# Kernel tuning notes

Measured on AMD Instinct MI355X. Metric: run time of the kernel, lower is better.

## Reference

```python
import jax, jax.numpy as jnp
import numpy as np
import math

B, T, C, H = 2, 2048, 512, 8
K, DIL = 3, 1
EPS = 1e-5


def _ln(x, g, b):
    m = jnp.mean(x, axis=-1, keepdims=True)
    v = jnp.mean(jnp.square(x - m), axis=-1, keepdims=True)
    return (x - m) * jax.lax.rsqrt(v + EPS) * g + b


def setup_inputs() -> dict:
    key = jax.random.key(0)
    ks = jax.random.split(key, 12)
    s = 0.02
    return {
        "x": jax.random.normal(ks[0], (B, T, C), jnp.float32),
        "conv_w": jax.random.normal(ks[1], (C, C, K), jnp.float32) * s,  # OIH
        "conv_b": jax.random.normal(ks[2], (C,), jnp.float32) * s,
        "g1": jnp.ones((C,), jnp.float32), "b1": jnp.zeros((C,), jnp.float32),
        "qkv_w": jax.random.normal(ks[3], (C, 3 * C), jnp.float32) * s,
        "qkv_b": jax.random.normal(ks[4], (3 * C,), jnp.float32) * s,
        "proj_w": jax.random.normal(ks[5], (C, C), jnp.float32) * s,
        "proj_b": jax.random.normal(ks[6], (C,), jnp.float32) * s,
        "g2": jnp.ones((C,), jnp.float32), "b2": jnp.zeros((C,), jnp.float32),
        "ffn_w1": jax.random.normal(ks[7], (C, 2 * C), jnp.float32) * s,
        "ffn_b1": jax.random.normal(ks[8], (2 * C,), jnp.float32) * s,
        "ffn_w2": jax.random.normal(ks[9], (2 * C, C), jnp.float32) * s,
        "ffn_b2": jax.random.normal(ks[10], (C,), jnp.float32) * s,
        "g3": jnp.ones((C,), jnp.float32), "b3": jnp.zeros((C,), jnp.float32),
    }


def reference(x, conv_w, conv_b, g1, b1, qkv_w, qkv_b, proj_w, proj_b,
              g2, b2, ffn_w1, ffn_b1, ffn_w2, ffn_b2, g3, b3):
    b, t, c = x.shape
    hd = c // H
    # --- causal dilated conv (left-pad only == pad both + right-trim) ---
    pad = (K - 1) * DIL
    xc = jnp.transpose(x, (0, 2, 1))  # [B,C,T]
    conv = jax.lax.conv_general_dilated(
        xc, conv_w, window_strides=(1,), padding=[(pad, 0)],
        rhs_dilation=(DIL,), dimension_numbers=("NCH", "OIH", "NCH"))
    conv = conv + conv_b[None, :, None]
    x = _ln(x + jnp.transpose(conv, (0, 2, 1)), g1, b1)
    # --- causal self-attention ---
    qkv = (x @ qkv_w + qkv_b).reshape(b, t, 3, H, hd)
    qkv = jnp.transpose(qkv, (2, 0, 3, 1, 4))  # [3,B,H,T,hd]
    q, k, v = qkv[0], qkv[1], qkv[2]
    scores = jnp.einsum("bhqd,bhkd->bhqk", q, k) / math.sqrt(hd)
    causal = jnp.tril(jnp.ones((t, t), bool))
    scores = jnp.where(causal, scores, -jnp.inf)
    attn = jax.nn.softmax(scores, axis=-1)
    out = jnp.einsum("bhqk,bhkd->bhqd", attn, v)
    out = jnp.transpose(out, (0, 2, 1, 3)).reshape(b, t, c)
    out = out @ proj_w + proj_b
    x = _ln(x + out, g2, b2)
    # --- FFN ---
    ffn = jax.nn.relu(x @ ffn_w1 + ffn_b1) @ ffn_w2 + ffn_b2
    return _ln(x + ffn, g3, b3)
```

## Files before the change

### kernel.cpp

```cpp
#include <hip/hip_runtime.h>
#include <hip/hip_bf16.h>

#define TT 2048
#define QSC 0.18033688011112042f

typedef __attribute__((ext_vector_type(4))) float f32x4;
typedef __attribute__((ext_vector_type(8))) __bf16 bf16x8;
typedef __attribute__((ext_vector_type(4))) short short4v;
typedef __attribute__((ext_vector_type(8))) short short8v;

enum { M_CONV = 0, M_QKV = 1, M_PROJ = 2, M_FFN1 = 3, M_FFN2 = 4 };

__device__ __forceinline__ void gload16(const void* g, void* l) {
    __builtin_amdgcn_global_load_lds(
        (__attribute__((address_space(1))) void*)g,
        (__attribute__((address_space(3))) void*)l, 16, 0, 0);
}

__device__ __forceinline__ short f2bf(float f) {
    unsigned u = __float_as_uint(f);
    u = (u + 0x7fffu + ((u >> 16) & 1u)) >> 16;
    return (short)u;
}

__device__ __forceinline__ float bf2f(short s) {
    unsigned u = ((unsigned)(unsigned short)s) << 16;
    return __uint_as_float(u);
}

__global__ __launch_bounds__(256) void prep_all(
    const float* __restrict__ conv_w, const float* __restrict__ x,
    const float* __restrict__ qkv_w, const float* __restrict__ proj_w,
    const float* __restrict__ f1w, const float* __restrict__ f2w,
    short* __restrict__ cwT, short* __restrict__ xpad,
    short* __restrict__ qkvT, short* __restrict__ projT,
    short* __restrict__ f1T, short* __restrict__ f2T) {
    if (blockIdx.x < 2048) {
        int t = blockIdx.x;
        const float* src; short* dst; int K, N, lt;
        if (t < 768)       { src = qkv_w;  dst = qkvT;  K = 512;  N = 1536; lt = t; }
        else if (t < 1024) { src = proj_w; dst = projT; K = 512;  N = 512;  lt = t - 768; }
        else if (t < 1536) { src = f1w;    dst = f1T;   K = 512;  N = 1024; lt = t - 1024; }
        else               { src = f2w;    dst = f2T;   K = 1024; N = 512;  lt = t - 1536; }
        int ntn = N >> 5;
        int kt = lt / ntn, nt = lt - kt * ntn;
        int k0 = kt * 32, n0 = nt * 32;
        __shared__ float tile[32][33];
        int c = threadIdx.x & 31, r = threadIdx.x >> 5;
        #pragma unroll
        for (int i = 0; i < 4; i++)
            tile[r + i * 8][c] = src[(size_t)(k0 + r + i * 8) * N + n0 + c];
        __syncthreads();
        #pragma unroll
        for (int i = 0; i < 4; i++)
            dst[(size_t)(n0 + r + i * 8) * K + k0 + c] = f2bf(tile[c][r + i * 8]);
        return;
    }
    if (blockIdx.x < 3072) {
        int oi = (blockIdx.x - 2048) * 256 + threadIdx.x;
        int o = oi >> 9, i = oi & 511;
        const float* s = conv_w + (size_t)oi * 3;
        #pragma unroll
        for (int tap = 0; tap < 3; tap++)
            cwT[(size_t)o * 1536 + tap * 512 + i] = f2bf(s[tap]);
        return;
    }
    int idx = (blockIdx.x - 3072) * 256 + threadIdx.x;
    int rp = idx >> 6, j = idx & 63;
    if (rp < 4100) {
        int bb = rp / 2050, rr = rp - bb * 2050;
        int t = rr - 2;
        short8v pk;
        if (t >= 0) {
            const float* xs = x + ((size_t)(bb << 11) + t) * 512 + j * 8;
            f32x4 a = *(const f32x4*)xs;
            f32x4 b2 = *(const f32x4*)(xs + 4);
            #pragma unroll
            for (int i = 0; i < 4; i++) { pk[i] = f2bf(a[i]); pk[i + 4] = f2bf(b2[i]); }
        } else {
            #pragma unroll
            for (int i = 0; i < 8; i++) pk[i] = 0;
        }
        *(short8v*)&xpad[(size_t)rp * 512 + j * 8] = pk;
    }
}

__global__ __launch_bounds__(512) void ln_row(const short* __restrict__ in,
                                              const float* __restrict__ g,
                                              const float* __restrict__ b,
                                              float* __restrict__ outf,
                                              short* __restrict__ outb) {
    int row = blockIdx.x * 8 + (threadIdx.x >> 6);
    int l = threadIdx.x & 63;
    short8v v = *(const short8v*)(in + (size_t)row * 512 + l * 8);
    float vf[8];
    float s = 0.f, ss = 0.f;
    #pragma unroll
    for (int i = 0; i < 8; i++) {
        vf[i] = bf2f(v[i]);
        s += vf[i]; ss += vf[i] * vf[i];
    }
    #pragma unroll
    for (int off = 1; off < 64; off <<= 1) {
        s  += __shfl_xor(s, off);
        ss += __shfl_xor(ss, off);
    }
    float mean = s * (1.f / 512);
    float var  = ss * (1.f / 512) - mean * mean;
    float rstd = rsqrtf(var + 1e-5f);
    f32x4 g0 = *(const f32x4*)(g + l * 8), g1 = *(const f32x4*)(g + l * 8 + 4);
    f32x4 b0 = *(const f32x4*)(b + l * 8), b1 = *(const f32x4*)(b + l * 8 + 4);
    float ov[8];
    #pragma unroll
    for (int i = 0; i < 4; i++) {
        ov[i]     = (vf[i]     - mean) * rstd * g0[i] + b0[i];
        ov[i + 4] = (vf[i + 4] - mean) * rstd * g1[i] + b1[i];
    }
    if (outf) {
        float* q = outf + (size_t)row * 512 + l * 8;
        *(f32x4*)q       = (f32x4){ov[0], ov[1], ov[2], ov[3]};
        *(f32x4*)(q + 4) = (f32x4){ov[4], ov[5], ov[6], ov[7]};
    }
    if (outb) {
        short8v pk;
        #pragma unroll
        for (int i = 0; i < 8; i++) pk[i] = f2bf(ov[i]);
        *(short8v*)(outb + (size_t)row * 512 + l * 8) = pk;
    }
}

template<int MODE>
__device__ __forceinline__ const short* a_ptr(const short* A, int m0, int r, int kk, int K) {
    if constexpr (MODE == M_CONV) {
        int row = m0 + r;
        int bb = row >> 11, t5 = row & 2047;
        int tap = kk >> 9, k2 = kk & 511;
        return A + ((size_t)(bb * 2050 + t5 + tap) * 512 + k2);
    } else {
        return A + ((size_t)(m0 + r) * K + kk);
    }
}

template<int MODE, int BM>
__global__ __launch_bounds__((BM == 64) ? 128 : 256) void gemm_mfma(
    const short* __restrict__ A, const short* __restrict__ Bw,
    const float* __restrict__ bias, const void* __restrict__ res,
    void* __restrict__ Cout, short* __restrict__ vTb,
    const float* __restrict__ pML, int K) {
    constexpr int NT  = (BM == 64) ? 128 : 256;
    constexpr int MF  = (BM == 64) ? 2 : 4;
    constexpr int NF  = (BM == 64) ? 4 : 2;
    constexpr int BCH = (BM == 64) ? 4 : 2;
    __shared__ short As[BM * 64];
    __shared__ short Bs[64 * 64];
    const int tid = threadIdx.x;
    const int w = tid >> 6, l = tid & 63;
    const int lr = l & 15, lc = l >> 4;
    const int wrb = (BM == 64) ? (w * 32) : ((w >> 1) * 64);
    const int wcb = (BM == 64) ? 0 : ((w & 1) * 32);
    const int m0 = blockIdx.x * BM, n0 = blockIdx.y * 64;
    f32x4 acc[MF][NF];
    #pragma unroll
    for (int mf = 0; mf < MF; mf++)
        #pragma unroll
        for (int nf = 0; nf < NF; nf++) acc[mf][nf] = (f32x4){0.f, 0.f, 0.f, 0.f};

    for (int k0 = 0; k0 < K; k0 += 64) {
        if constexpr (MODE == M_PROJ) {
            const int bq = blockIdx.x >> 5, qt = blockIdx.x & 31;
            const int h = k0 >> 6;
            const int Lb = ((31 - qt) << 5) | (bq * 8 + h);
            #pragma unroll
            for (int i = 0; i < 4; i++) {
                int u = i * NT + tid, r = u >> 3, c = (u & 7) ^ (r & 7);
                float m0_ = pML[(size_t)Lb * 128 + r];
                float l0_ = pML[(size_t)Lb * 128 + 64 + r];
                float m1_ = pML[(size_t)(Lb | 16) * 128 + r];
                float l1_ = pML[(size_t)(Lb | 16) * 128 + 64 + r];
                float mn = fmaxf(m0_, m1_);
                float a0 = exp2f(m0_ - mn), a1 = exp2f(m1_ - mn);
                float inv = 1.f / (l0_ * a0 + l1_ * a1);
                short8v o0 = *(const short8v*)&A[(size_t)Lb * 4096 + r * 64 + c * 8];
                short8v o1 = *(const short8v*)&A[(size_t)(Lb | 16) * 4096 + r * 64 + c * 8];
                short8v mv;
                #pragma unroll
                for (int j = 0; j < 8; j++)
                    mv[j] = f2bf((bf2f(o0[j]) * a0 + bf2f(o1[j]) * a1) * inv);
                *(short8v*)((char*)As + u * 16) = mv;
            }
            #pragma unroll
            for (int i = 0; i < BCH; i++) {
                int u = i * NT + tid, r = u >> 3, c = (u & 7) ^ (r & 7);
                gload16(Bw + ((size_t)(n0 + r) * K + k0 + c * 8), (char*)Bs + u * 16);
            }
        } else {
            #pragma unroll
            for (int i = 0; i < 4; i++) {
                int u = i * NT + tid, r = u >> 3, c = (u & 7) ^ (r & 7);
                gload16(a_ptr<MODE>(A, m0, r, k0 + c * 8, K), (char*)As + u * 16);
            }
            #pragma unroll
            for (int i = 0; i < BCH; i++) {
                int u = i * NT + tid, r = u >> 3, c = (u & 7) ^ (r & 7);
                gload16(Bw + ((size_t)(n0 + r) * K + k0 + c * 8), (char*)Bs + u * 16);
            }
        }
        __syncthreads();
        bf16x8 af[MF][2], bfv[NF][2];
        #pragma unroll
        for (int mf = 0; mf < MF; mf++)
            #pragma unroll
            for (int ks = 0; ks < 2; ks++) {
                int rr = wrb + mf * 16 + lr;
                int cc = (ks * 4 + lc) ^ (rr & 7);
                af[mf][ks] = *(const bf16x8*)&As[rr * 64 + cc * 8];
            }
        #pragma unroll
        for (int nf = 0; nf < NF; nf++)
            #pragma unroll
            for (int ks = 0; ks < 2; ks++) {
                int rr = wcb + nf * 16 + lr;
                int cc = (ks * 4 + lc) ^ (rr & 7);
                bfv[nf][ks] = *(const bf16x8*)&Bs[rr * 64 + cc * 8];
            }
        __builtin_amdgcn_s_setprio(1);
        #pragma unroll
        for (int nf = 0; nf < NF; nf++)
            #pragma unroll
            for (int ks = 0; ks < 2; ks++)
                #pragma unroll
                for (int mf = 0; mf < MF; mf++)
                    acc[mf][nf] = __builtin_amdgcn_mfma_f32_16x16x32_bf16(
                        af[mf][ks], bfv[nf][ks], acc[mf][nf], 0, 0, 0);
        __builtin_amdgcn_s_setprio(0);
        __syncthreads();
    }
    #pragma unroll
    for (int mf = 0; mf < MF; mf++) {
        int row0 = m0 + wrb + mf * 16 + lc * 4;
        #pragma unroll
        for (int nf = 0; nf < NF; nf++) {
            int col = n0 + wcb + nf * 16 + lr;
            float bv = bias[col];
            if constexpr (MODE == M_CONV) {
                short* Cb = (short*)Cout;
                const float* rf = (const float*)res;
                #pragma unroll
                for (int rg = 0; rg < 4; rg++) {
                    size_t off = (size_t)(row0 + rg) * 512 + col;
                    Cb[off] = f2bf(acc[mf][nf][rg] + bv + rf[off]);
                }
            } else if constexpr (MODE == M_PROJ || MODE == M_FFN2) {
                short* Cb = (short*)Cout;
                const short* rb = (const short*)res;
                #pragma unroll
                for (int rg = 0; rg < 4; rg++) {
                    size_t off = (size_t)(row0 + rg) * 512 + col;
                    Cb[off] = f2bf(acc[mf][nf][rg] + bv + bf2f(rb[off]));
                }
            } else if constexpr (MODE == M_FFN1) {
                short* Cb = (short*)Cout;
                #pragma unroll
                for (int rg = 0; rg < 4; rg++)
                    Cb[(size_t)(row0 + rg) * 1024 + col] =
                        f2bf(fmaxf(acc[mf][nf][rg] + bv, 0.f));
            } else {
                short* Cb = (short*)Cout;
                float v[4];
                #pragma unroll
                for (int rg = 0; rg < 4; rg++) {
                    v[rg] = acc[mf][nf][rg] + bv;
                    float wv = (col < 512) ? v[rg] * QSC : v[rg];
                    Cb[(size_t)(row0 + rg) * 1536 + col] = f2bf(wv);
                }
                if (col >= 1024) {
                    int vc = col - 1024, hh = vc >> 6, dd = vc & 63;
                    int bb = row0 >> 11, t5 = row0 & 2047;
                    short4v pk = {f2bf(v[0]), f2bf(v[1]), f2bf(v[2]), f2bf(v[3])};
                    *(short4v*)&vTb[((size_t)((bb << 3) + hh) * 64 + dd) * 2048 + t5] = pk;
                }
            }
        }
    }
}

__global__ __launch_bounds__(256) void attn_part(const short* __restrict__ qkvb,
                                                 const short* __restrict__ vTb,
                                                 short* __restrict__ pO,
                                                 float* __restrict__ pML) {
    __shared__ short SM[20992];
    __bf16* SMb = (__bf16*)SM;
    const int tid = threadIdx.x;
    const int w = tid >> 6, l = tid & 63;
    const int lr = l & 15, lc = l >> 4;
    const int L = blockIdx.x;
    const int bh = L & 15;
    const int par = (L >> 4) & 1;
    const int qt = 31 - (L >> 5);
    const int b = bh >> 3, h = bh & 7;
    const int qr = w * 16, q0 = qt * 64;
    const int pbase = 16384 + w * (16 * 72);
    const int ntiles = (qt >= par) ? ((qt - par) >> 1) + 1 : 0;

    #pragma unroll
    for (int i = 0; i < 2; i++) {
        int u = i * 256 + tid, r = u >> 3, c = (u & 7) ^ (r & 7);
        gload16(qkvb + ((size_t)(b * 2048 + q0 + r) * 1536 + h * 64 + c * 8),
                (char*)&SM[16384] + u * 16);
        if (ntiles > 0) {
            gload16(qkvb + ((size_t)(b * 2048 + par * 64 + r) * 1536 + 512 + h * 64 + c * 8),
                    (char*)&SM[0] + u * 16);
            gload16(vTb + ((size_t)(bh * 64 + r) * 2048 + par * 64 + c * 8),
                    (char*)&SM[8192] + u * 16);
        }
    }
    __syncthreads();
    bf16x8 aq[2];
    #pragma unroll
    for (int ks = 0; ks < 2; ks++) {
        int rr = qr + lr;
        int cc = (lc + 4 * ks) ^ (rr & 7);
        aq[ks] = *(const bf16x8*)&SM[16384 + rr * 64 + cc * 8];
    }
    __syncthreads();

    bf16x8 onesf;
    #pragma unroll
    for (int i = 0; i < 8; i++) onesf[i] = (__bf16)1.0f;

    f32x4 o[4], lacc;
    float mst[4];
    #pragma unroll
    for (int nf = 0; nf < 4; nf++) o[nf] = (f32x4){0.f, 0.f, 0.f, 0.f};
    lacc = (f32x4){0.f, 0.f, 0.f, 0.f};
    #pragma unroll
    for (int rg = 0; rg < 4; rg++) mst[rg] = -1e30f;

    for (int s = 0; s < ntiles; s++) {
        const int kt = par + 2 * s;
        const int cur = s & 1;
        if (s + 1 < ntiles) {
            int ktn = kt + 2, nb = (cur ^ 1) * 4096;
            #pragma unroll
            for (int i = 0; i < 2; i++) {
                int u = i * 256 + tid, r = u >> 3, c = (u & 7) ^ (r & 7);
                gload16(qkvb + ((size_t)(b * 2048 + ktn * 64 + r) * 1536 + 512 + h * 64 + c * 8),
                        (char*)&SM[nb] + u * 16);
                gload16(vTb + ((size_t)(bh * 64 + r) * 2048 + ktn * 64 + c * 8),
                        (char*)&SM[8192 + nb] + u * 16);
            }
        }
        f32x4 s4[4];
        #pragma unroll
        for (int nf = 0; nf < 4; nf++) s4[nf] = (f32x4){0.f, 0.f, 0.f, 0.f};
        __builtin_amdgcn_s_setprio(1);
        #pragma unroll
        for (int nf = 0; nf < 4; nf++) {
            #pragma unroll
            for (int ks = 0; ks < 2; ks++) {
                int rr = nf * 16 + lr;
                int cc = (lc + 4 * ks) ^ (rr & 7);
                bf16x8 bk = *(const bf16x8*)&SM[cur * 4096 + rr * 64 + cc * 8];
                s4[nf] = __builtin_amdgcn_mfma_f32_16x16x32_bf16(aq[ks], bk, s4[nf], 0, 0, 0);
            }
        }
        __builtin_amdgcn_s_setprio(0);
        const bool diag = (kt == qt);
        if (diag) {
            #pragma unroll
            for (int nf = 0; nf < 4; nf++)
                #pragma unroll
                for (int rg = 0; rg < 4; rg++)
                    if (nf * 16 + lr > qr + lc * 4 + rg) s4[nf][rg] = -1e30f;
        }
        float rm[4];
        int ok = 1;
        #pragma unroll
        for (int rg = 0; rg < 4; rg++) {
            float m_ = fmaxf(fmaxf(s4[0][rg], s4[1][rg]), fmaxf(s4[2][rg], s4[3][rg]));
            m_ = fmaxf(m_, __shfl_xor(m_, 1));
            m_ = fmaxf(m_, __shfl_xor(m_, 2));
            m_ = fmaxf(m_, __shfl_xor(m_, 4));
            m_ = fmaxf(m_, __shfl_xor(m_, 8));
            rm[rg] = m_;
            ok &= (m_ <= mst[rg] + 11.5f);
        }
        if (!__all(ok)) {
            #pragma unroll
            for (int rg = 0; rg < 4; rg++) {
                float mn = fmaxf(mst[rg], rm[rg]);
                float alpha = exp2f(mst[rg] - mn);
                mst[rg] = mn;
                lacc[rg] *= alpha;
                #pragma unroll
                for (int nf = 0; nf < 4; nf++) o[nf][rg] *= alpha;
            }
        }
        #pragma unroll
        for (int rg = 0; rg < 4; rg++) {
            int prow = pbase + (lc * 4 + rg) * 72;
            SMb[prow      + lr] = (__bf16)exp2f(s4[0][rg] - mst[rg]);
            SMb[prow + 16 + lr] = (__bf16)exp2f(s4[1][rg] - mst[rg]);
            SMb[prow + 32 + lr] = (__bf16)exp2f(s4[2][rg] - mst[rg]);
            SMb[prow + 48 + lr] = (__bf16)exp2f(s4[3][rg] - mst[rg]);
        }
        bf16x8 pa[2];
        #pragma unroll
        for (int ks = 0; ks < 2; ks++)
            pa[ks] = *(const bf16x8*)&SM[pbase + lr * 72 + ks * 32 + lc * 8];
        __builtin_amdgcn_s_setprio(1);
        #pragma unroll
        for (int ks = 0; ks < 2; ks++)
            lacc = __builtin_amdgcn_mfma_f32_16x16x32_bf16(pa[ks], onesf, lacc, 0, 0, 0);
        #pragma unroll
        for (int nf = 0; nf < 4; nf++) {
            #pragma unroll
            for (int ks = 0; ks < 2; ks++) {
                int rr = nf * 16 + lr;
                int cc = (lc + 4 * ks) ^ (rr & 7);
                bf16x8 bv = *(const bf16x8*)&SM[8192 + cur * 4096 + rr * 64 + cc * 8];
                o[nf] = __builtin_amdgcn_mfma_f32_16x16x32_bf16(pa[ks], bv, o[nf], 0, 0, 0);
            }
        }
        __builtin_amdgcn_s_setprio(0);
        __syncthreads();
    }

    size_t ob = (size_t)L * 4096;
    #pragma unroll
    for (int nf = 0; nf < 4; nf++) {
        #pragma unroll
        for (int rg = 0; rg < 4; rg++) {
            int rw = qr + lc * 4 + rg;
            pO[ob + rw * 64 + nf * 16 + lr] = (ntiles > 0) ? f2bf(o[nf][rg]) : (short)0;
        }
    }
    if (lr == 0) {
        #pragma unroll
        for (int rg = 0; rg < 4; rg++) {
            int rw = qr + lc * 4 + rg;
            pML[(size_t)L * 128 + rw]      = (ntiles > 0) ? mst[rg] : -1e30f;
            pML[(size_t)L * 128 + 64 + rw] = (ntiles > 0) ? lacc[rg] : 0.f;
        }
    }
}

extern "C" void kernel_launch(void* const* d_in, const int* in_sizes, int n_in,
                              void* d_out, int out_size, void* d_ws, size_t ws_size,
                              hipStream_t stream) {
    const float* x      = (const float*)d_in[0];
    const float* conv_w = (const float*)d_in[1];
    const float* conv_b = (const float*)d_in[2];
    const float* g1     = (const float*)d_in[3];
    const float* b1     = (const float*)d_in[4];
    const float* qkv_w  = (const float*)d_in[5];
    const float* qkv_b  = (const float*)d_in[6];
    const float* proj_w = (const float*)d_in[7];
    const float* proj_b = (const float*)d_in[8];
    const float* g2     = (const float*)d_in[9];
    const float* b2     = (const float*)d_in[10];
    const float* ffn_w1 = (const float*)d_in[11];
    const float* ffn_b1 = (const float*)d_in[12];
    const float* ffn_w2 = (const float*)d_in[13];
    const float* ffn_b2 = (const float*)d_in[14];
    const float* g3     = (const float*)d_in[15];
    const float* b3     = (const float*)d_in[16];
    float* out = (float*)d_out;

    char* p = (char*)d_ws;
    short* cwT   = (short*)p;  p += 786432 * 2;
    short* qkvT  = (short*)p;  p += 786432 * 2;
    short* projT = (short*)p;  p += 262144 * 2;
    short* f1T   = (short*)p;  p += 524288 * 2;
    short* f2T   = (short*)p;  p += 524288 * 2;
    short* xpad  = (short*)p;  p += 2099200 * 2;
    short* yb    = (short*)p;  p += 2097152 * 2;
    short* x1b   = (short*)p;  p += 2097152 * 2;
    short* qkvb  = (short*)p;  p += 6291456 * 2;
    short* vTb   = (short*)p;  p += 2097152 * 2;
    short* pO    = (short*)p;  p += 4194304 * 2;
    float* pML   = (float*)p;  p += 131072 * 4;
    short* x2b = x1b;
    short* hb  = qkvb;

    prep_all<<<4097, 256, 0, stream>>>(conv_w, x, qkv_w, proj_w, ffn_w1, ffn_w2,
                                       cwT, xpad, qkvT, projT, f1T, f2T);
    gemm_mfma<M_CONV, 64><<<dim3(64, 8), 128, 0, stream>>>(
        xpad, cwT, conv_b, x, yb, nullptr, nullptr, 1536);
    ln_row<<<512, 512, 0, stream>>>(yb, g1, b1, nullptr, x1b);
    gemm_mfma<M_QKV, 128><<<dim3(32, 24), 256, 0, stream>>>(
        x1b, qkvT, qkv_b, nullptr, qkvb, vTb, nullptr, 512);
    attn_part<<<1024, 256, 0, stream>>>(qkvb, vTb, pO, pML);
    gemm_mfma<M_PROJ, 64><<<dim3(64, 8), 128, 0, stream>>>(
        pO, projT, proj_b, x1b, yb, nullptr, pML, 512);
    ln_row<<<512, 512, 0, stream>>>(yb, g2, b2, nullptr, x2b);
    gemm_mfma<M_FFN1, 128><<<dim3(32, 16), 256, 0, stream>>>(
        x2b, f1T, ffn_b1, nullptr, hb, nullptr, nullptr, 512);
    gemm_mfma<M_FFN2, 64><<<dim3(64, 8), 128, 0, stream>>>(
        hb, f2T, ffn_b2, x2b, yb, nullptr, nullptr, 1024);
    ln_row<<<512, 512, 0, stream>>>(yb, g3, b3, out, nullptr);
}
```

Measured before the change: 128.2 us.

## Split attention keys four ways with separate merge kernel; narrow N tiles

Attention now splits each query tile's key range into four interleaved partitions instead of two. That doubles the grid to 2048 blocks and shortens the longest per-block loop. A new attn_merge kernel combines the four partials into a plain bf16 attention output, replacing the merge that was fused into the projection GEMM's A-load. The 64-row GEMMs (conv, proj, ffn2) use BN=32 tiles with twice as many column blocks to raise occupancy. The costs are an extra launch, double the partial-output traffic, and more redundant A loads across the narrower tiles.

```diff
diff --git a/kernel.cpp b/kernel.cpp
--- a/kernel.cpp
+++ b/kernel.cpp
@@ -141,24 +141,24 @@
     }
 }
 
-template<int MODE, int BM>
+template<int MODE, int BM, int BN>
 __global__ __launch_bounds__((BM == 64) ? 128 : 256) void gemm_mfma(
     const short* __restrict__ A, const short* __restrict__ Bw,
     const float* __restrict__ bias, const void* __restrict__ res,
-    void* __restrict__ Cout, short* __restrict__ vTb,
-    const float* __restrict__ pML, int K) {
+    void* __restrict__ Cout, short* __restrict__ vTb, int K) {
     constexpr int NT  = (BM == 64) ? 128 : 256;
     constexpr int MF  = (BM == 64) ? 2 : 4;
-    constexpr int NF  = (BM == 64) ? 4 : 2;
-    constexpr int BCH = (BM == 64) ? 4 : 2;
+    constexpr int NF  = 2;
+    constexpr int ACH = (BM * 64 * 2) / (16 * NT);
+    constexpr int BCH = (BN * 64 * 2) / (16 * NT);
     __shared__ short As[BM * 64];
-    __shared__ short Bs[64 * 64];
+    __shared__ short Bs[BN * 64];
     const int tid = threadIdx.x;
     const int w = tid >> 6, l = tid & 63;
     const int lr = l & 15, lc = l >> 4;
     const int wrb = (BM == 64) ? (w * 32) : ((w >> 1) * 64);
     const int wcb = (BM == 64) ? 0 : ((w & 1) * 32);
-    const int m0 = blockIdx.x * BM, n0 = blockIdx.y * 64;
+    const int m0 = blockIdx.x * BM, n0 = blockIdx.y * BN;
     f32x4 acc[MF][NF];
     #pragma unroll
     for (int mf = 0; mf < MF; mf++)
@@ -166,44 +166,15 @@
         for (int nf = 0; nf < NF; nf++) acc[mf][nf] = (f32x4){0.f, 0.f, 0.f, 0.f};
 
     for (int k0 = 0; k0 < K; k0 += 64) {
-        if constexpr (MODE == M_PROJ) {
-            const int bq = blockIdx.x >> 5, qt = blockIdx.x & 31;
-            const int h = k0 >> 6;
-            const int Lb = ((31 - qt) << 5) | (bq * 8 + h);
-            #pragma unroll
-            for (int i = 0; i < 4; i++) {
-                int u = i * NT + tid, r = u >> 3, c = (u & 7) ^ (r & 7);
-                float m0_ = pML[(size_t)Lb * 128 + r];
-                float l0_ = pML[(size_t)Lb * 128 + 64 + r];
-                float m1_ = pML[(size_t)(Lb | 16) * 128 + r];
-                float l1_ = pML[(size_t)(Lb | 16) * 128 + 64 + r];
-                float mn = fmaxf(m0_, m1_);
-                float a0 = exp2f(m0_ - mn), a1 = exp2f(m1_ - mn);
-                float inv = 1.f / (l0_ * a0 + l1_ * a1);
-                short8v o0 = *(const short8v*)&A[(size_t)Lb * 4096 + r * 64 + c * 8];
-                short8v o1 = *(const short8v*)&A[(size_t)(Lb | 16) * 4096 + r * 64 + c * 8];
-                short8v mv;
-                #pragma unroll
-                for (int j = 0; j < 8; j++)
-                    mv[j] = f2bf((bf2f(o0[j]) * a0 + bf2f(o1[j]) * a1) * inv);
-                *(short8v*)((char*)As + u * 16) = mv;
-            }
-            #pragma unroll
-            for (int i = 0; i < BCH; i++) {
-                int u = i * NT + tid, r = u >> 3, c = (u & 7) ^ (r & 7);
-                gload16(Bw + ((size_t)(n0 + r) * K + k0 + c * 8), (char*)Bs + u * 16);
-            }
-        } else {
-            #pragma unroll
-            for (int i = 0; i < 4; i++) {
-                int u = i * NT + tid, r = u >> 3, c = (u & 7) ^ (r & 7);
-                gload16(a_ptr<MODE>(A, m0, r, k0 + c * 8, K), (char*)As + u * 16);
-            }
-            #pragma unroll
-            for (int i = 0; i < BCH; i++) {
-                int u = i * NT + tid, r = u >> 3, c = (u & 7) ^ (r & 7);
-                gload16(Bw + ((size_t)(n0 + r) * K + k0 + c * 8), (char*)Bs + u * 16);
-            }
+        #pragma unroll
+        for (int i = 0; i < ACH; i++) {
+            int u = i * NT + tid, r = u >> 3, c = (u & 7) ^ (r & 7);
+            gload16(a_ptr<MODE>(A, m0, r, k0 + c * 8, K), (char*)As + u * 16);
+        }
+        #pragma unroll
+        for (int i = 0; i < BCH; i++) {
+            int u = i * NT + tid, r = u >> 3, c = (u & 7) ^ (r & 7);
+            gload16(Bw + ((size_t)(n0 + r) * K + k0 + c * 8), (char*)Bs + u * 16);
         }
         __syncthreads();
         bf16x8 af[MF][2], bfv[NF][2];
@@ -295,12 +266,12 @@
     const int lr = l & 15, lc = l >> 4;
     const int L = blockIdx.x;
     const int bh = L & 15;
-    const int par = (L >> 4) & 1;
-    const int qt = 31 - (L >> 5);
+    const int par = (L >> 4) & 3;
+    const int qt = 31 - (L >> 6);
     const int b = bh >> 3, h = bh & 7;
     const int qr = w * 16, q0 = qt * 64;
     const int pbase = 16384 + w * (16 * 72);
-    const int ntiles = (qt >= par) ? ((qt - par) >> 1) + 1 : 0;
+    const int ntiles = (qt >= par) ? ((qt - par) >> 2) + 1 : 0;
 
     #pragma unroll
     for (int i = 0; i < 2; i++) {
@@ -337,10 +308,10 @@
     for (int rg = 0; rg < 4; rg++) mst[rg] = -1e30f;
 
     for (int s = 0; s < ntiles; s++) {
-        const int kt = par + 2 * s;
+        const int kt = par + 4 * s;
         const int cur = s & 1;
         if (s + 1 < ntiles) {
-            int ktn = kt + 2, nb = (cur ^ 1) * 4096;
+            int ktn = kt + 4, nb = (cur ^ 1) * 4096;
             #pragma unroll
             for (int i = 0; i < 2; i++) {
                 int u = i * 256 + tid, r = u >> 3, c = (u & 7) ^ (r & 7);
@@ -442,6 +413,45 @@
             pML[(size_t)L * 128 + rw]      = (ntiles > 0) ? mst[rg] : -1e30f;
             pML[(size_t)L * 128 + 64 + rw] = (ntiles > 0) ? lacc[rg] : 0.f;
         }
+    }
+}
+
+__global__ __launch_bounds__(256) void attn_merge(const short* __restrict__ pO,
+                                                  const float* __restrict__ pML,
+                                                  short* __restrict__ aout) {
+    int U = blockIdx.x;
+    int bh = U & 15, qt = U >> 4;
+    int b = bh >> 3, h = bh & 7, q0 = qt * 64;
+    int Lb = ((31 - qt) << 6) | bh;
+    int t = threadIdx.x;
+    int r = t >> 2, cs = (t & 3) * 16;
+    float m[4], lv[4];
+    #pragma unroll
+    for (int pp = 0; pp < 4; pp++) {
+        m[pp]  = pML[(size_t)(Lb | (pp << 4)) * 128 + r];
+        lv[pp] = pML[(size_t)(Lb | (pp << 4)) * 128 + 64 + r];
+    }
+    float mn = fmaxf(fmaxf(m[0], m[1]), fmaxf(m[2], m[3]));
+    float a[4], den = 0.f;
+    #pragma unroll
+    for (int pp = 0; pp < 4; pp++) { a[pp] = exp2f(m[pp] - mn); den += lv[pp] * a[pp]; }
+    float inv = 1.f / den;
+    #pragma unroll
+    for (int half = 0; half < 2; half++) {
+        int c0 = cs + half * 8;
+        float accv[8];
+        #pragma unroll
+        for (int j = 0; j < 8; j++) accv[j] = 0.f;
+        #pragma unroll
+        for (int pp = 0; pp < 4; pp++) {
+            short8v ov = *(const short8v*)&pO[(size_t)(Lb | (pp << 4)) * 4096 + r * 64 + c0];
+            #pragma unroll
+            for (int j = 0; j < 8; j++) accv[j] += bf2f(ov[j]) * a[pp];
+        }
+        short8v res;
+        #pragma unroll
+        for (int j = 0; j < 8; j++) res[j] = f2bf(accv[j] * inv);
+        *(short8v*)&aout[(size_t)(b * 2048 + q0 + r) * 512 + h * 64 + c0] = res;
     }
 }
 
@@ -478,25 +488,27 @@
     short* x1b   = (short*)p;  p += 2097152 * 2;
     short* qkvb  = (short*)p;  p += 6291456 * 2;
     short* vTb   = (short*)p;  p += 2097152 * 2;
-    short* pO    = (short*)p;  p += 4194304 * 2;
-    float* pML   = (float*)p;  p += 131072 * 4;
-    short* x2b = x1b;
-    short* hb  = qkvb;
+    short* pO    = (short*)p;  p += 8388608 * 2;
+    float* pML   = (float*)p;  p += 262144 * 4;
+    short* x2b     = x1b;
+    short* hb      = qkvb;
+    short* attnout = xpad;
 
     prep_all<<<4097, 256, 0, stream>>>(conv_w, x, qkv_w, proj_w, ffn_w1, ffn_w2,
                                        cwT, xpad, qkvT, projT, f1T, f2T);
-    gemm_mfma<M_CONV, 64><<<dim3(64, 8), 128, 0, stream>>>(
-        xpad, cwT, conv_b, x, yb, nullptr, nullptr, 1536);
+    gemm_mfma<M_CONV, 64, 32><<<dim3(64, 16), 128, 0, stream>>>(
+        xpad, cwT, conv_b, x, yb, nullptr, 1536);
     ln_row<<<512, 512, 0, stream>>>(yb, g1, b1, nullptr, x1b);
-    gemm_mfma<M_QKV, 128><<<dim3(32, 24), 256, 0, stream>>>(
-        x1b, qkvT, qkv_b, nullptr, qkvb, vTb, nullptr, 512);
-    attn_part<<<1024, 256, 0, stream>>>(qkvb, vTb, pO, pML);
-    gemm_mfma<M_PROJ, 64><<<dim3(64, 8), 128, 0, stream>>>(
-        pO, projT, proj_b, x1b, yb, nullptr, pML, 512);
+    gemm_mfma<M_QKV, 128, 64><<<dim3(32, 24), 256, 0, stream>>>(
+        x1b, qkvT, qkv_b, nullptr, qkvb, vTb, 512);
+    attn_part<<<2048, 256, 0, stream>>>(qkvb, vTb, pO, pML);
+    attn_merge<<<512, 256, 0, stream>>>(pO, pML, attnout);
+    gemm_mfma<M_PROJ, 64, 32><<<dim3(64, 16), 128, 0, stream>>>(
+        attnout, projT, proj_b, x1b, yb, nullptr, 512);
     ln_row<<<512, 512, 0, stream>>>(yb, g2, b2, nullptr, x2b);
-    gemm_mfma<M_FFN1, 128><<<dim3(32, 16), 256, 0, stream>>>(
-        x2b, f1T, ffn_b1, nullptr, hb, nullptr, nullptr, 512);
-    gemm_mfma<M_FFN2, 64><<<dim3(64, 8), 128, 0, stream>>>(
-        hb, f2T, ffn_b2, x2b, yb, nullptr, nullptr, 1024);
+    gemm_mfma<M_FFN1, 128, 64><<<dim3(32, 16), 256, 0, stream>>>(
+        x2b, f1T, ffn_b1, nullptr, hb, nullptr, 512);
+    gemm_mfma<M_FFN2, 64, 32><<<dim3(64, 16), 128, 0, stream>>>(
+        hb, f2T, ffn_b2, x2b, yb, nullptr, 1024);
     ln_row<<<512, 512, 0, stream>>>(yb, g3, b3, out, nullptr);
 }
```

Result: faster. 119.4 us (-6.9%).
